# Kernel optimization log

Hardware: AMD Instinct MI355X
Metric: run time of the kernel (lower is better)

## Reference

```python
import jax
import jax.numpy as jnp
import numpy as np
from jax import lax
from jax.scipy.special import logsumexp

B, T, D = 8, 512, 768
S, H, O = 8, 32, 32
TRANS_W, EMISS_W = 0.5, 0.5


def setup_inputs() -> dict:
    key = jax.random.key(0)
    ks = jax.random.split(key, 8)
    emb = jax.random.normal(ks[0], (B, T, D), dtype=jnp.float32)
    u = jax.random.uniform(ks[1], (B, T, S, O), minval=1e-3, maxval=1.0)
    obs = (u / u.sum(-1, keepdims=True)).astype(jnp.float32)
    seq_lengths = jax.random.randint(ks[2], (B,), T // 2, T + 1).at[0].set(T).astype(jnp.int32)
    # HMM params (match torch init)
    priors = jnp.zeros(H).at[0].set(1.0) + jnp.full(H, 0.001).at[0].set(0.0)
    priors = jnp.full(H, 0.001).at[0].set(1.0)
    state_priors = jnp.log(priors)
    unnorm_trans = jax.random.normal(ks[3], (H, H))
    unnorm_emiss = jnp.zeros((S, H, O))
    # xavier_uniform with relu gain
    gain = np.sqrt(2.0)
    a_t = gain * np.sqrt(6.0 / (D + H * H))
    Wt = jax.random.uniform(ks[4], (D, H * H), minval=-a_t, maxval=a_t)
    bt = jnp.zeros(H * H)
    a_e = gain * np.sqrt(6.0 / (D + H * O))
    We = jax.random.uniform(ks[5], (S, D, H * O), minval=-a_e, maxval=a_e)
    be = jnp.zeros((S, H * O))
    return {"emb": emb, "obs": obs, "seq_lengths": seq_lengths,
            "state_priors": state_priors, "unnorm_trans": unnorm_trans,
            "unnorm_emiss": unnorm_emiss, "Wt": Wt, "bt": bt, "We": We, "be": be}


def _chmm_forward(emb, obs, state_priors, unnorm_trans, unnorm_emiss, Wt, bt, We, be, seq_lengths):
    b, t, d = emb.shape
    s, h, o = unnorm_emiss.shape
    lsp = jax.nn.log_softmax(state_priors)                               # [H]
    trans = jax.nn.softmax(unnorm_trans, axis=-1)                        # [H,H]
    emiss = jax.nn.softmax(unnorm_emiss, axis=-1)                        # [S,H,O]
    nn_trans = jax.nn.softmax((emb @ Wt + bt).reshape(b, t, h, h), axis=-1)
    nn_emiss = jax.nn.softmax((jnp.einsum('btd,sde->btse', emb, We) + be).reshape(b, t, s, h, o), axis=-1)
    log_trans = jnp.log((1.0 - TRANS_W) * trans + TRANS_W * nn_trans)    # [B,T,H,H]
    log_emiss = jnp.log((1.0 - EMISS_W) * emiss + EMISS_W * nn_emiss)    # [B,T,S,H,O]

    # normalize_observation: replace non-observing sources on entity positions
    lbs = jnp.argmax(obs, axis=-1)                                       # [B,T,S]
    entity = lbs.sum(-1) > 0                                             # [B,T]
    no_ent = lbs == 0                                                    # [B,T,S]
    mask = entity[:, :, None] & no_ent
    subst = jnp.full((o,), 0.99 / o).at[0].set(0.01)
    obs = jnp.where(mask[..., None], subst, obs)

    # log emission probs: logsumexp over obs dim, sum over sources -> [B,T,H]
    lep = logsumexp(log_emiss + jnp.log(obs)[:, :, :, None, :], axis=-1).sum(axis=2)

    # forward recursion (normalized alpha), scan over time
    a0 = lsp + lep[:, 0]
    a0 = a0 - logsumexp(a0, axis=-1, keepdims=True)
    lep_t = jnp.swapaxes(lep, 0, 1)          # [T,B,H]
    tr_t = jnp.swapaxes(log_trans, 0, 1)     # [T,B,H,H]

    def fstep(a, x):
        lep_i, tr_i = x
        la = lep_i + logsumexp(a[:, :, None] + tr_i, axis=1)
        la = la - logsumexp(la, axis=-1, keepdims=True)
        return la, la

    _, alphas = lax.scan(fstep, a0, (lep_t[1:], tr_t[1:]))
    log_alpha = jnp.swapaxes(jnp.concatenate([a0[None], alphas], 0), 0, 1)   # [B,T,H]

    # backward recursion (reverse scan); uses lep at time t (faithful to source)
    def bstep(bv, x):
        lep_i, tr_i = x
        nb = logsumexp(tr_i + (lep_i + bv)[:, None, :], axis=-1)
        return nb, nb

    _, betas = lax.scan(bstep, jnp.zeros((b, h)), (lep_t[:-1], tr_t[:-1]), reverse=True)
    log_beta = jnp.swapaxes(jnp.concatenate([betas, jnp.zeros((1, b, h))], 0), 0, 1)  # [B,T,H]
    shifts = seq_lengths - t
    log_beta = jax.vmap(lambda bb, ss: jnp.roll(bb, ss, axis=0))(log_beta, shifts)

    log_gamma = log_alpha + log_beta
    ng = log_gamma - logsumexp(log_gamma, axis=-1, keepdims=True)
    # xi for t = 1..T-1 (vectorized, no recursion)
    xi = log_trans[:, 1:] + log_alpha[:, :-1, :, None] + (lep[:, 1:] + log_beta[:, 1:])[:, :, None, :]
    xi = xi - logsumexp(xi.reshape(b, t - 1, -1), axis=-1)[..., None, None]

    log_prior = (jnp.exp(ng[:, 0]) * lsp).sum(-1).mean()
    tran_terms = (jnp.exp(xi) * log_trans[:, 1:]).sum((-2, -1))          # [B,T-1]
    t1 = jnp.arange(t - 1)[None, :]
    log_tran = jnp.where(t1 < (seq_lengths - 1)[:, None], tran_terms, 0.0).sum(-1).mean()
    emis_terms = (jnp.exp(ng) * lep).sum(-1)                             # [B,T]
    t2 = jnp.arange(t)[None, :]
    log_emis = jnp.where(t2 < seq_lengths[:, None], emis_terms, 0.0).sum(-1).mean()
    ll = log_prior + log_tran + log_emis
    return ll, log_trans, log_emiss


def reference(emb, obs, seq_lengths, state_priors, unnorm_trans, unnorm_emiss, Wt, bt, We, be):
    return _chmm_forward(emb, obs, state_priors, unnorm_trans, unnorm_emiss, Wt, bt, We, be, seq_lengths)
```

## Files before the change

### kernel.cpp

```cpp
#include <hip/hip_runtime.h>
#include <hip/hip_bf16.h>


typedef __attribute__((ext_vector_type(8))) short bf16x8;
typedef __attribute__((ext_vector_type(4))) float f32x4;

#define B_MBF   0
#define B_LDOT  16777216
#define B_CHNK  16777216
#define B_ABND  18874368
#define B_BBND  18907136
#define B_PART  18939904
#define B_LEP   20971520
#define B_ELEP  21496064
#define B_ALIN  22020352
#define B_BLIN  22544640
#define B_TRSM  23068928
#define B_EMSM  23073024
#define B_OBSM  23105792
#define B_ABF   27447552
#define B_WTBF  33739008

#define OUT_TR_BASE 1
#define OUT_EM_BASE 4194305

__device__ __forceinline__ float wsum32(float v) {
#pragma unroll
  for (int m = 16; m >= 1; m >>= 1) v += __shfl_xor(v, m);
  return v;
}
__device__ __forceinline__ float wmax32(float v) {
#pragma unroll
  for (int m = 16; m >= 1; m >>= 1) v = fmaxf(v, __shfl_xor(v, m));
  return v;
}
__device__ __forceinline__ short f2bf(float f) {
  union { float f; unsigned int u; } c; c.f = f;
  unsigned int u = c.u;
  unsigned int r = (u + 0x7FFFu + ((u >> 16) & 1u)) >> 16;
  return (short)r;
}
__device__ __forceinline__ float bf2f(short h) {
  union { unsigned int u; float f; } c;
  c.u = ((unsigned int)(unsigned short)h) << 16;
  return c.f;
}
__device__ __forceinline__ void gload16(const void* g, void* l) {
  __builtin_amdgcn_global_load_lds(
      (const __attribute__((address_space(1))) unsigned int*)g,
      (__attribute__((address_space(3))) unsigned int*)l, 16, 0, 0);
}

__global__ __launch_bounds__(256) void k_prep(
    const float* __restrict__ emb, short* __restrict__ Abf,
    const float* __restrict__ Wt, const float* __restrict__ We,
    short* __restrict__ WT,
    const float* __restrict__ ut, const float* __restrict__ ue,
    float* __restrict__ tsm, float* __restrict__ esm,
    const float* __restrict__ obs, float* __restrict__ om) {
  __shared__ float tile[32][33];
  __shared__ int lbs_s[8];
  __shared__ int entf;
  const int blk = blockIdx.x;
  const int tid = threadIdx.x;
  if (blk < 3072) {
    const int idx = (blk * 256 + tid) * 4;
#pragma unroll
    for (int c = 0; c < 4; ++c) Abf[idx + c] = f2bf(emb[idx + c]);
  } else if (blk < 9984) {
    const int x = blk - 3072;
    const int nb = (x % 288) * 32, kb = (x / 288) * 32;
    const int tx = tid & 31, ty = tid >> 5;
#pragma unroll
    for (int ii = 0; ii < 4; ++ii) {
      const int k = kb + ty + ii * 8;
      const int n = nb + tx;
      float v;
      if (n < 1024) v = Wt[(size_t)k * 1024 + n];
      else {
        const int ne = n - 1024, s = ne >> 10, c = ne & 1023;
        v = We[((size_t)s * 768 + k) * 1024 + c];
      }
      tile[ty + ii * 8][tx] = v;
    }
    __syncthreads();
#pragma unroll
    for (int ii = 0; ii < 4; ++ii) {
      const int n = nb + ty + ii * 8;
      const int k = kb + tx;
      WT[(size_t)n * 768 + k] = f2bf(tile[tx][ty + ii * 8]);
    }
  } else if (blk < 14080) {
    const int bt = blk - 9984;
    const int o = tid & 31;
    const float v = obs[((size_t)bt << 8) + tid];
    float bv = v; int am = o;
#pragma unroll
    for (int m = 16; m >= 1; m >>= 1) {
      const float ov_ = __shfl_xor(bv, m);
      const int oa = __shfl_xor(am, m);
      if (ov_ > bv || (ov_ == bv && oa < am)) { bv = ov_; am = oa; }
    }
    if (o == 0) lbs_s[tid >> 5] = am;
    __syncthreads();
    if (tid == 0) {
      int e = 0;
#pragma unroll
      for (int s = 0; s < 8; ++s) e += lbs_s[s];
      entf = (e > 0) ? 1 : 0;
    }
    __syncthreads();
    const bool msk = entf && (lbs_s[tid >> 5] == 0);
    const float sub = (o == 0) ? 0.01f : (0.99f / 32.0f);
    om[((size_t)bt << 8) + tid] = msk ? sub : v;
  } else {
    const int row = (blk - 14080) * 8 + (tid >> 5);
    const int j = tid & 31;
    const float* src; float* dst;
    if (row < 32) { src = ut + row * 32; dst = tsm + row * 32; }
    else          { src = ue + (row - 32) * 32; dst = esm + (row - 32) * 32; }
    float v = src[j];
    float mx = wmax32(v);
    float e = __expf(v - mx);
    float s = wsum32(e);
    dst[j] = e / s;
  }
}

#define BM 128
#define BN 128
#define BK 64

__global__ __launch_bounds__(512, 4) void gemm_epi(
    const short* __restrict__ A, const short* __restrict__ WT,
    const float* __restrict__ btb, const float* __restrict__ beb,
    const float* __restrict__ tsm, const float* __restrict__ esm,
    const float* __restrict__ om,
    float* __restrict__ out, short* __restrict__ Mbf, float* __restrict__ ldot) {
  __shared__ __align__(16) char smem[32768];
  short* lsA = (short*)smem;
  short* lsB = (short*)(smem + 16384);
  float* lsOm = (float*)smem;

  const int bid = blockIdx.x;
  const int xcd = bid & 7;
  const int local = bid >> 3;
  const int ntile = xcd * 9 + (local % 9);
  const int mtile = local / 9;
  const int m0 = mtile * BM;
  const int n0 = ntile * BN;

  const int tid = threadIdx.x;
  const int lane = tid & 63;
  const int w = tid >> 6;
  const int wr = w >> 1, wc = w & 1;
  const int l15 = lane & 15, lq = lane >> 4;

  const int lr = lane >> 3;
  const int lc = (lane & 7) ^ lr;
  const short* gA = A + (size_t)(m0 + (w << 3) + lr) * 768 + (lc << 3);
  const short* gB = WT + (size_t)(n0 + (w << 3) + lr) * 768 + (lc << 3);
  const int lofs = (w << 10) + (lane << 4);
  char* lA = (char*)lsA + lofs;
  char* lB = (char*)lsB + lofs;

  f32x4 acc[2][4] = {};

  for (int kt = 0; kt < 768; kt += BK) {
#pragma unroll
    for (int it = 0; it < 2; ++it) {
      gload16(gA + it * (64 * 768) + kt, lA + (it << 13));
      gload16(gB + it * (64 * 768) + kt, lB + (it << 13));
    }
    __syncthreads();
#pragma unroll
    for (int kk = 0; kk < 2; ++kk) {
      const int kbyte = kk * 64 + lq * 16;
      bf16x8 af[2], bfr[4];
#pragma unroll
      for (int mi = 0; mi < 2; ++mi) {
        const int m = wr * 32 + mi * 16 + l15;
        af[mi] = *(const bf16x8*)((const char*)lsA + ((m * 128 + kbyte) ^ ((m & 7) << 4)));
      }
#pragma unroll
      for (int ni = 0; ni < 4; ++ni) {
        const int n = wc * 64 + ni * 16 + l15;
        bfr[ni] = *(const bf16x8*)((const char*)lsB + ((n * 128 + kbyte) ^ ((n & 7) << 4)));
      }
#pragma unroll
      for (int mi = 0; mi < 2; ++mi)
#pragma unroll
        for (int ni = 0; ni < 4; ++ni)
          acc[mi][ni] = __builtin_amdgcn_mfma_f32_16x16x32_bf16(af[mi], bfr[ni], acc[mi][ni], 0, 0, 0);
    }
    __syncthreads();
  }

  const bool isem = (n0 >= 1024);
  int sblk = 0;
  if (isem) {
    sblk = (n0 - 1024) >> 10;
    const int row = tid >> 2, part = (tid & 3) << 3;
    const float* src = om + (((size_t)(m0 + row)) << 8) + (sblk << 5) + part;
    float* dst = lsOm + row * 36 + part;
    *(float4*)dst = *(const float4*)src;
    *(float4*)(dst + 4) = *(const float4*)(src + 4);
    __syncthreads();
  }

#pragma unroll
  for (int g = 0; g < 2; ++g) {
    const int nbase = n0 + wc * 64 + g * 32;
    const int c0 = nbase + l15;
    const int c1 = c0 + 16;
    const float bias0 = isem ? beb[c0 - 1024] : btb[c0];
    const float bias1 = isem ? beb[c1 - 1024] : btb[c1];
    const float base0 = isem ? esm[c0 - 1024] : tsm[c0];
    const float base1 = isem ? esm[c1 - 1024] : tsm[c1];
    const int h = (nbase >> 5) & 31;
#pragma unroll
    for (int mi = 0; mi < 2; ++mi) {
      const int rl0 = wr * 32 + mi * 16 + lq * 4;
      const int rowb = m0 + rl0;
      float e0[4], e1[4], sm[4];
#pragma unroll
      for (int r = 0; r < 4; ++r) {
        e0[r] = __expf(acc[mi][2 * g][r] + bias0);
        e1[r] = __expf(acc[mi][2 * g + 1][r] + bias1);
        sm[r] = e0[r] + e1[r];
      }
#pragma unroll
      for (int m_ = 1; m_ < 16; m_ <<= 1) {
#pragma unroll
        for (int r = 0; r < 4; ++r) sm[r] += __shfl_xor(sm[r], m_);
      }
      float M0[4], M1[4], lg0[4], lg1[4];
#pragma unroll
      for (int r = 0; r < 4; ++r) {
        const float inv = 0.5f * __builtin_amdgcn_rcpf(sm[r]);
        M0[r] = 0.5f * base0 + e0[r] * inv;
        M1[r] = 0.5f * base1 + e1[r] * inv;
        lg0[r] = __logf(M0[r]);
        lg1[r] = __logf(M1[r]);
      }
      if (!isem) {
#pragma unroll
        for (int r = 0; r < 4; ++r) {
          const size_t rb = ((size_t)(rowb + r)) << 10;
          out[OUT_TR_BASE + rb + c0] = lg0[r];
          out[OUT_TR_BASE + rb + c1] = lg1[r];
          Mbf[rb + c0] = f2bf(M0[r]);
          Mbf[rb + c1] = f2bf(M1[r]);
        }
      } else {
        const int ne0 = c0 - 1024;
        float dt[4];
#pragma unroll
        for (int r = 0; r < 4; ++r) {
          const float* ov = lsOm + (rl0 + r) * 36;
          dt[r] = M0[r] * ov[l15] + M1[r] * ov[l15 + 16];
        }
#pragma unroll
        for (int m_ = 1; m_ < 16; m_ <<= 1) {
#pragma unroll
          for (int r = 0; r < 4; ++r) dt[r] += __shfl_xor(dt[r], m_);
        }
#pragma unroll
        for (int r = 0; r < 4; ++r) {
          const size_t rb = ((size_t)(rowb + r)) << 13;
          out[OUT_EM_BASE + rb + ne0] = lg0[r];
          out[OUT_EM_BASE + rb + ne0 + 16] = lg1[r];
        }
        if (l15 == 0) {
#pragma unroll
          for (int r = 0; r < 4; ++r)
            ldot[(((size_t)(rowb + r)) << 8) + (sblk << 5) + h] = __logf(dt[r]);
        }
      }
    }
  }
}

__global__ __launch_bounds__(64) void k_elep(const float* __restrict__ ldot,
                                             float* __restrict__ lep,
                                             float* __restrict__ elep) {
  const int bt = blockIdx.x;
  const int l = threadIdx.x, i = l & 31;
  const float* ld = ldot + ((size_t)bt << 8);
  float v = 0.f;
#pragma unroll
  for (int s = 0; s < 8; ++s) v += ld[(s << 5) + i];
  float mx = wmax32(v);
  if (l < 32) {
    lep[((size_t)bt << 5) + i] = v;
    elep[((size_t)bt << 5) + i] = __expf(v - mx);
  }
}

__global__ __launch_bounds__(256) void k_chunk(const short* __restrict__ Mbf,
                                               const float* __restrict__ elep,
                                               float* __restrict__ chnk) {
  const int blk = blockIdx.x;
  const int dir = blk >> 8;
  const int b = (blk >> 5) & 7, c = blk & 31;
  int t0, t1;
  if (dir == 0) { t0 = 16 * c + 1; t1 = 16 * c + 16; if (t1 > 511) t1 = 511; }
  else          { t0 = 16 * c;     t1 = 16 * c + 15; if (t1 > 510) t1 = 510; }
  const size_t base = (size_t)b << 9;
  __shared__ float Pl[1024];
  __shared__ float Gl[1024];
  __shared__ float red[4];
  const int tid = threadIdx.x;
  const int r = tid >> 3;
  const int cq = (tid & 7) << 2;
  float4 p;
  {
    const short4 mh = *(const short4*)(Mbf + ((base + t0) << 10) + (tid << 2));
    const float4 e = *(const float4*)(elep + ((base + t0) << 5) + cq);
    p.x = bf2f(mh.x) * e.x; p.y = bf2f(mh.y) * e.y;
    p.z = bf2f(mh.z) * e.z; p.w = bf2f(mh.w) * e.w;
  }
  for (int t = t0 + 1; t <= t1; ++t) {
    *(float4*)(Pl + (tid << 2)) = p;
    const short4 mh = *(const short4*)(Mbf + ((base + t) << 10) + (tid << 2));
    const float4 e = *(const float4*)(elep + ((base + t) << 5) + cq);
    float4 g;
    g.x = bf2f(mh.x) * e.x; g.y = bf2f(mh.y) * e.y;
    g.z = bf2f(mh.z) * e.z; g.w = bf2f(mh.w) * e.w;
    *(float4*)(Gl + (tid << 2)) = g;
    __syncthreads();
    float4 nv = {0.f, 0.f, 0.f, 0.f};
#pragma unroll
    for (int j = 0; j < 32; ++j) {
      const float pr = Pl[(r << 5) + j];
      const float4 gj = *(const float4*)(Gl + (j << 5) + cq);
      nv.x = fmaf(pr, gj.x, nv.x);
      nv.y = fmaf(pr, gj.y, nv.y);
      nv.z = fmaf(pr, gj.z, nv.z);
      nv.w = fmaf(pr, gj.w, nv.w);
    }
    float mx = fmaxf(fmaxf(nv.x, nv.y), fmaxf(nv.z, nv.w));
#pragma unroll
    for (int mm = 32; mm >= 1; mm >>= 1) mx = fmaxf(mx, __shfl_xor(mx, mm));
    if ((tid & 63) == 0) red[tid >> 6] = mx;
    __syncthreads();
    mx = fmaxf(fmaxf(red[0], red[1]), fmaxf(red[2], red[3]));
    const float rs = __builtin_amdgcn_rcpf(mx);
    p.x = nv.x * rs; p.y = nv.y * rs; p.z = nv.z * rs; p.w = nv.w * rs;
  }
  *(float4*)(chnk + ((size_t)blk << 10) + (tid << 2)) = p;
}

__global__ __launch_bounds__(64) void k_stitch(const float* __restrict__ chnk,
                                               const float* __restrict__ elep,
                                               const float* __restrict__ sp,
                                               float* __restrict__ ab,
                                               float* __restrict__ bb) {
  const int l = threadIdx.x, i = l & 31, half = l >> 5;
  const int bid = blockIdx.x;
  const int b = bid & 7;
  float v;
  float pb0[16], pb1[16];
  if (bid < 8) {
    const float* base = chnk + ((size_t)(b << 5) << 10);
    auto LDP = [&](float (&pb)[16], int c) {
      const float* P = base + ((size_t)c << 10) + ((half << 4) << 5) + i;
#pragma unroll
      for (int jj = 0; jj < 16; ++jj) pb[jj] = P[jj << 5];
    };
    auto STEP = [&](float (&pb)[16], int c) {
      float pj[16];
#pragma unroll
      for (int jj = 0; jj < 16; ++jj) pj[jj] = __shfl(v, (half << 4) + jj);
      float a0 = 0.f, a1 = 0.f, a2 = 0.f, a3 = 0.f;
#pragma unroll
      for (int q = 0; q < 4; ++q) {
        a0 = fmaf(pj[(q << 2) + 0], pb[(q << 2) + 0], a0);
        a1 = fmaf(pj[(q << 2) + 1], pb[(q << 2) + 1], a1);
        a2 = fmaf(pj[(q << 2) + 2], pb[(q << 2) + 2], a2);
        a3 = fmaf(pj[(q << 2) + 3], pb[(q << 2) + 3], a3);
      }
      float av = (a0 + a1) + (a2 + a3);
      av += __shfl_xor(av, 32);
      const float S = wsum32(av);
      v = av * __builtin_amdgcn_rcpf(S);
      if (l < 32) ab[(((b << 5) + (c + 1)) << 5) + i] = v;
    };
    {
      float u = sp[i];
      float mx = wmax32(u);
      float pe = __expf(u - mx);
      float s = wsum32(pe);
      v = (pe / s) * elep[((size_t)(b << 9) << 5) + i];
      float S = wsum32(v);
      v /= S;
      if (l < 32) ab[((b << 5) << 5) + i] = v;
    }
    LDP(pb0, 0);
    int c = 0;
    for (; c + 1 <= 30; c += 2) {
      LDP(pb1, c + 1);
      STEP(pb0, c);
      LDP(pb0, (c + 2 <= 30) ? c + 2 : 30);
      STEP(pb1, c + 1);
    }
    if (c == 30) STEP(pb0, 30);
  } else {
    const float* base = chnk + ((size_t)(256 + (b << 5)) << 10);
    auto LDP = [&](float (&pb)[16], int c) {
      const float4* P = (const float4*)(base + ((size_t)c << 10) + (i << 5) + (half << 4));
#pragma unroll
      for (int q = 0; q < 4; ++q) {
        const float4 x = P[q];
        pb[(q << 2) + 0] = x.x; pb[(q << 2) + 1] = x.y;
        pb[(q << 2) + 2] = x.z; pb[(q << 2) + 3] = x.w;
      }
    };
    auto STEP = [&](float (&pb)[16], int c) {
      float qj[16];
#pragma unroll
      for (int jj = 0; jj < 16; ++jj) qj[jj] = __shfl(v, (half << 4) + jj);
      float a0 = 0.f, a1 = 0.f, a2 = 0.f, a3 = 0.f;
#pragma unroll
      for (int q = 0; q < 4; ++q) {
        a0 = fmaf(qj[(q << 2) + 0], pb[(q << 2) + 0], a0);
        a1 = fmaf(qj[(q << 2) + 1], pb[(q << 2) + 1], a1);
        a2 = fmaf(qj[(q << 2) + 2], pb[(q << 2) + 2], a2);
        a3 = fmaf(qj[(q << 2) + 3], pb[(q << 2) + 3], a3);
      }
      float av = (a0 + a1) + (a2 + a3);
      av += __shfl_xor(av, 32);
      const float S = wsum32(av);
      v = av * __builtin_amdgcn_rcpf(S);
      if (l < 32) bb[(((b << 5) + c) << 5) + i] = v;
    };
    v = 1.0f / 32.0f;
    LDP(pb0, 31);
    int c = 31;
    for (; c - 1 >= 1; c -= 2) {
      LDP(pb1, c - 1);
      STEP(pb0, c);
      LDP(pb0, (c - 2 >= 1) ? c - 2 : 1);
      STEP(pb1, c - 1);
    }
    if (c == 1) STEP(pb0, 1);
  }
}

__global__ __launch_bounds__(64) void k_recon(const short* __restrict__ Mbf,
                                              const float* __restrict__ elep,
                                              const float* __restrict__ ab,
                                              const float* __restrict__ bb,
                                              float* __restrict__ alin,
                                              float* __restrict__ blin) {
  const int l = threadIdx.x, i = l & 31, half = l >> 5;
  const int blk = blockIdx.x;
  const int dir = blk >> 8;
  const int b = (blk >> 5) & 7, c = blk & 31;
  const size_t base = (size_t)b << 9;
  const short* Mb = Mbf + (base << 10);
  const float* Eb = elep + (base << 5);
  float v;
  float m0[16], m1[16];
  float e0, e1;
  if (dir == 0) {
    float* Ab = alin + (base << 5);
    const int cb = ((half << 4) << 5) + i;
    auto LDF = [&](float (&mb)[16], float& eb, int t) {
      const short* Mr = Mb + ((size_t)t << 10) + cb;
#pragma unroll
      for (int jj = 0; jj < 16; ++jj) mb[jj] = bf2f(Mr[jj << 5]);
      eb = Eb[(t << 5) + i];
    };
    auto STEPF = [&](float (&mb)[16], float eb, int t) {
      float pj[16];
#pragma unroll
      for (int jj = 0; jj < 16; ++jj) pj[jj] = __shfl(v, (half << 4) + jj);
      float a0 = 0.f, a1 = 0.f, a2 = 0.f, a3 = 0.f;
#pragma unroll
      for (int q = 0; q < 4; ++q) {
        a0 = fmaf(pj[(q << 2) + 0], mb[(q << 2) + 0], a0);
        a1 = fmaf(pj[(q << 2) + 1], mb[(q << 2) + 1], a1);
        a2 = fmaf(pj[(q << 2) + 2], mb[(q << 2) + 2], a2);
        a3 = fmaf(pj[(q << 2) + 3], mb[(q << 2) + 3], a3);
      }
      float av = (a0 + a1) + (a2 + a3);
      av += __shfl_xor(av, 32);
      const float nv = av * eb;
      const float S = wsum32(nv);
      v = nv * __builtin_amdgcn_rcpf(S);
      if (l < 32) Ab[(t << 5) + i] = v;
    };
    v = ab[(((b << 5) + c) << 5) + i];
    const int t0 = c << 4;
    if (l < 32) Ab[(t0 << 5) + i] = v;
    const int te = t0 + 15;
    LDF(m0, e0, t0 + 1);
    int t = t0 + 1;
    for (; t + 1 <= te; t += 2) {
      LDF(m1, e1, t + 1);
      STEPF(m0, e0, t);
      LDF(m0, e0, (t + 2 <= te) ? t + 2 : te);
      STEPF(m1, e1, t + 1);
    }
    if (t == te) STEPF(m0, e0, t);
  } else {
    float* Bb = blin + (base << 5);
    auto LDB = [&](float (&mb)[16], float& eb, int t) {
      const short4* Mr = (const short4*)(Mb + ((size_t)t << 10) + (i << 5) + (half << 4));
#pragma unroll
      for (int q = 0; q < 4; ++q) {
        const short4 x = Mr[q];
        mb[(q << 2) + 0] = bf2f(x.x); mb[(q << 2) + 1] = bf2f(x.y);
        mb[(q << 2) + 2] = bf2f(x.z); mb[(q << 2) + 3] = bf2f(x.w);
      }
      eb = Eb[(t << 5) + i];
    };
    auto STEPB = [&](float (&mb)[16], float eb, int t) {
      const float q0 = v * eb;
      float qj[16];
#pragma unroll
      for (int jj = 0; jj < 16; ++jj) qj[jj] = __shfl(q0, (half << 4) + jj);
      float a0 = 0.f, a1 = 0.f, a2 = 0.f, a3 = 0.f;
#pragma unroll
      for (int q = 0; q < 4; ++q) {
        a0 = fmaf(qj[(q << 2) + 0], mb[(q << 2) + 0], a0);
        a1 = fmaf(qj[(q << 2) + 1], mb[(q << 2) + 1], a1);
        a2 = fmaf(qj[(q << 2) + 2], mb[(q << 2) + 2], a2);
        a3 = fmaf(qj[(q << 2) + 3], mb[(q << 2) + 3], a3);
      }
      float av = (a0 + a1) + (a2 + a3);
      av += __shfl_xor(av, 32);
      const float S = wsum32(av);
      v = av * __builtin_amdgcn_rcpf(S);
      if (l < 32) Bb[(t << 5) + i] = v;
    };
    int ts;
    if (c == 31) {
      v = 1.0f / 32.0f;
      if (l < 32) Bb[(511 << 5) + i] = v;
      ts = 510;
    } else {
      v = bb[(((b << 5) + (c + 1)) << 5) + i];
      ts = (c << 4) + 15;
    }
    const int te = c << 4;
    LDB(m0, e0, ts);
    int t = ts;
    for (; t - 1 >= te; t -= 2) {
      LDB(m1, e1, t - 1);
      STEPB(m0, e0, t);
      LDB(m0, e0, (t - 2 >= te) ? t - 2 : te);
      STEPB(m1, e1, t - 1);
    }
    if (t == te) STEPB(m0, e0, t);
  }
}

__global__ __launch_bounds__(64) void k_final(
    const float* __restrict__ out_log,
    const float* __restrict__ alin, const float* __restrict__ blin,
    const float* __restrict__ elep, const float* __restrict__ lep,
    const int* __restrict__ seqlen, const float* __restrict__ sp,
    float* __restrict__ part) {
  const int bt = blockIdx.x;
  const int b = bt >> 9, t = bt & 511;
  const int l = threadIdx.x, i = l & 31;
  const int L = seqlen[b];
  const int tb = (t + 512 - L) & 511;
  const float a = alin[((size_t)bt << 5) + i];
  const float br = blin[((((size_t)b << 9) + tb) << 5) + i];
  const float g = a * br;
  float Z = wsum32(g);
  Z = fmaxf(Z, 1e-37f);
  const float ng = g / Z;
  const float es = wsum32(ng * lep[((size_t)bt << 5) + i]);
  float pr = 0.0f;
  if (t == 0) {
    const float v = sp[i];
    const float mx = wmax32(v);
    const float pe = __expf(v - mx);
    const float ss = wsum32(pe);
    const float lsp = v - mx - __logf(ss);
    pr = wsum32(ng * lsp);
  }
  float tran = 0.0f;
  if (t >= 1) {
    const float u = elep[((size_t)bt << 5) + i] * br;
    const int jb = (l & 1) << 4;
    float uj[16];
#pragma unroll
    for (int jj = 0; jj < 16; ++jj) uj[jj] = __shfl(u, jb + jj);
    const float ap = alin[(((size_t)bt - 1) << 5) + (l >> 1)];
    const float* Lr = out_log + OUT_TR_BASE + ((size_t)bt << 10) + ((l >> 1) << 5) + jb;
    float accZ = 0.0f, accT = 0.0f;
#pragma unroll
    for (int c = 0; c < 16; ++c) {
      const float lv = Lr[c];
      const float wv = __expf(lv) * ap * uj[c];
      accZ += wv;
      accT = fmaf(wv, lv, accT);
    }
#pragma unroll
    for (int m_ = 32; m_ >= 1; m_ >>= 1) {
      accZ += __shfl_xor(accZ, m_);
      accT += __shfl_xor(accT, m_);
    }
    tran = accT / accZ;
  }
  if (l == 0) {
    part[bt * 3 + 0] = (t == 0) ? pr : 0.0f;
    part[bt * 3 + 1] = (t >= 1 && t < L) ? tran : 0.0f;
    part[bt * 3 + 2] = (t < L) ? es : 0.0f;
  }
}

__global__ __launch_bounds__(256) void k_ll(const float* __restrict__ part,
                                            float* __restrict__ out) {
  __shared__ float red[8];
  const int tid = threadIdx.x;
  const int b = tid >> 5, i = tid & 31;
  float s = 0.0f;
#pragma unroll
  for (int k = 0; k < 16; ++k) {
    const int bt = (b << 9) + (k << 5) + i;
    s += part[bt * 3 + 0] + part[bt * 3 + 1] + part[bt * 3 + 2];
  }
  s = wsum32(s);
  if (i == 0) red[b] = s;
  __syncthreads();
  if (tid == 0) {
    float v = 0.0f;
#pragma unroll
    for (int b2 = 0; b2 < 8; ++b2) v += red[b2];
    out[0] = v / 8.0f;
  }
}

extern "C" void kernel_launch(void* const* d_in, const int* in_sizes, int n_in,
                              void* d_out, int out_size, void* d_ws, size_t ws_size,
                              hipStream_t stream) {
  const float* emb    = (const float*)d_in[0];
  const float* obs    = (const float*)d_in[1];
  const int*   seqlen = (const int*)  d_in[2];
  const float* sp     = (const float*)d_in[3];
  const float* utr    = (const float*)d_in[4];
  const float* uem    = (const float*)d_in[5];
  const float* Wt     = (const float*)d_in[6];
  const float* btb    = (const float*)d_in[7];
  const float* We     = (const float*)d_in[8];
  const float* beb    = (const float*)d_in[9];
  float* out = (float*)d_out;
  char* ws = (char*)d_ws;

  short* Mbf  = (short*)(ws + B_MBF);
  float* ldot = (float*)(ws + B_LDOT);
  float* chnk = (float*)(ws + B_CHNK);
  float* abnd = (float*)(ws + B_ABND);
  float* bbnd = (float*)(ws + B_BBND);
  float* part = (float*)(ws + B_PART);
  float* lep  = (float*)(ws + B_LEP);
  float* elep = (float*)(ws + B_ELEP);
  float* alin = (float*)(ws + B_ALIN);
  float* blin = (float*)(ws + B_BLIN);
  float* tsm  = (float*)(ws + B_TRSM);
  float* esm  = (float*)(ws + B_EMSM);
  float* om   = (float*)(ws + B_OBSM);
  short* Abf  = (short*)(ws + B_ABF);
  short* WTbf = (short*)(ws + B_WTBF);

  k_prep<<<14116, 256, 0, stream>>>(emb, Abf, Wt, We, WTbf, utr, uem, tsm, esm,
                                    obs, om);
  gemm_epi<<<2304, 512, 0, stream>>>(Abf, WTbf, btb, beb, tsm, esm, om,
                                     out, Mbf, ldot);
  k_elep<<<4096, 64, 0, stream>>>(ldot, lep, elep);
  k_chunk<<<512, 256, 0, stream>>>(Mbf, elep, chnk);
  k_stitch<<<16, 64, 0, stream>>>(chnk, elep, sp, abnd, bbnd);
  k_recon<<<512, 64, 0, stream>>>(Mbf, elep, abnd, bbnd, alin, blin);
  k_final<<<4096, 64, 0, stream>>>(out, alin, blin, elep, lep, seqlen, sp, part);
  k_ll<<<1, 256, 0, stream>>>(part, out);
}
```

Baseline: 164.1 us.

## Triple-buffer GEMM K-loop with BK=32 and async prefetch two stages ahead

Replaces the single-buffered BK=64 GEMM main loop, which synchronized twice per iteration, with a three-stage LDS ring buffer using BK=32. Loads are issued two stages ahead, and a single barrier per step is guarded by explicit vmcnt waits. The LDS layout and swizzle are reworked so each half-tile row pair maps conflict-free, with offsets precomputed outside the loop. The aim is to overlap global-to-LDS copies with MFMA work. In exchange it uses 48KB of shared memory, which may limit occupancy, and it doubles the number of loop iterations.

```diff
diff --git a/kernel.cpp b/kernel.cpp
--- a/kernel.cpp
+++ b/kernel.cpp
@@ -129,7 +129,7 @@
 
 #define BM 128
 #define BN 128
-#define BK 64
+#define BK 32
 
 __global__ __launch_bounds__(512, 4) void gemm_epi(
     const short* __restrict__ A, const short* __restrict__ WT,
@@ -137,9 +137,7 @@
     const float* __restrict__ tsm, const float* __restrict__ esm,
     const float* __restrict__ om,
     float* __restrict__ out, short* __restrict__ Mbf, float* __restrict__ ldot) {
-  __shared__ __align__(16) char smem[32768];
-  short* lsA = (short*)smem;
-  short* lsB = (short*)(smem + 16384);
+  __shared__ __align__(16) char smem[49152];
   float* lsOm = (float*)smem;
 
   const int bid = blockIdx.x;
@@ -156,44 +154,60 @@
   const int wr = w >> 1, wc = w & 1;
   const int l15 = lane & 15, lq = lane >> 4;
 
-  const int lr = lane >> 3;
-  const int lc = (lane & 7) ^ lr;
-  const short* gA = A + (size_t)(m0 + (w << 3) + lr) * 768 + (lc << 3);
-  const short* gB = WT + (size_t)(n0 + (w << 3) + lr) * 768 + (lc << 3);
+  const int jh = (lane & 7) ^ (lane >> 3);
+  const int srow = (w << 4) + ((lane >> 3) << 1) + (jh & 1);
+  const int sc = jh >> 1;
+  const short* gA = A + (size_t)(m0 + srow) * 768 + (sc << 3);
+  const short* gB = WT + (size_t)(n0 + srow) * 768 + (sc << 3);
   const int lofs = (w << 10) + (lane << 4);
-  char* lA = (char*)lsA + lofs;
-  char* lB = (char*)lsB + lofs;
+
+  int offA[2], offB[4];
+#pragma unroll
+  for (int mi = 0; mi < 2; ++mi) {
+    const int r = wr * 32 + mi * 16 + l15;
+    offA[mi] = ((r >> 1) << 7) + (((((r & 1)) + (lq << 1)) ^ ((r >> 1) & 7)) << 4);
+  }
+#pragma unroll
+  for (int ni = 0; ni < 4; ++ni) {
+    const int r = wc * 64 + ni * 16 + l15;
+    offB[ni] = 8192 + (((r >> 1)) << 7) + ((((r & 1) + (lq << 1)) ^ ((r >> 1) & 7)) << 4);
+  }
 
   f32x4 acc[2][4] = {};
 
-  for (int kt = 0; kt < 768; kt += BK) {
-#pragma unroll
-    for (int it = 0; it < 2; ++it) {
-      gload16(gA + it * (64 * 768) + kt, lA + (it << 13));
-      gload16(gB + it * (64 * 768) + kt, lB + (it << 13));
-    }
-    __syncthreads();
-#pragma unroll
-    for (int kk = 0; kk < 2; ++kk) {
-      const int kbyte = kk * 64 + lq * 16;
-      bf16x8 af[2], bfr[4];
-#pragma unroll
-      for (int mi = 0; mi < 2; ++mi) {
-        const int m = wr * 32 + mi * 16 + l15;
-        af[mi] = *(const bf16x8*)((const char*)lsA + ((m * 128 + kbyte) ^ ((m & 7) << 4)));
-      }
-#pragma unroll
-      for (int ni = 0; ni < 4; ++ni) {
-        const int n = wc * 64 + ni * 16 + l15;
-        bfr[ni] = *(const bf16x8*)((const char*)lsB + ((n * 128 + kbyte) ^ ((n & 7) << 4)));
-      }
-#pragma unroll
-      for (int mi = 0; mi < 2; ++mi)
-#pragma unroll
-        for (int ni = 0; ni < 4; ++ni)
-          acc[mi][ni] = __builtin_amdgcn_mfma_f32_16x16x32_bf16(af[mi], bfr[ni], acc[mi][ni], 0, 0, 0);
-    }
-    __syncthreads();
+  auto STAGE = [&](int bi, int kt) {
+    char* d = smem + (bi << 14) + lofs;
+    gload16(gA + kt, d);
+    gload16(gB + kt, d + 8192);
+  };
+
+  STAGE(0, 0);
+  STAGE(1, 32);
+  asm volatile("s_waitcnt vmcnt(2)" ::: "memory");
+  __builtin_amdgcn_s_barrier();
+  __builtin_amdgcn_sched_barrier(0);
+
+  int b0 = 0, b1 = 1, b2 = 2;
+#pragma unroll 3
+  for (int it = 0; it < 24; ++it) {
+    if (it < 22) STAGE(b2, (it + 2) * 32);
+    const char* s = smem + (b0 << 14);
+    bf16x8 af[2], bfr[4];
+#pragma unroll
+    for (int mi = 0; mi < 2; ++mi) af[mi] = *(const bf16x8*)(s + offA[mi]);
+#pragma unroll
+    for (int ni = 0; ni < 4; ++ni) bfr[ni] = *(const bf16x8*)(s + offB[ni]);
+#pragma unroll
+    for (int mi = 0; mi < 2; ++mi)
+#pragma unroll
+      for (int ni = 0; ni < 4; ++ni)
+        acc[mi][ni] = __builtin_amdgcn_mfma_f32_16x16x32_bf16(af[mi], bfr[ni], acc[mi][ni], 0, 0, 0);
+    if (it < 22)      asm volatile("s_waitcnt vmcnt(2)" ::: "memory");
+    else if (it < 23) asm volatile("s_waitcnt vmcnt(0)" ::: "memory");
+    __builtin_amdgcn_sched_barrier(0);
+    __builtin_amdgcn_s_barrier();
+    __builtin_amdgcn_sched_barrier(0);
+    const int tb = b0; b0 = b1; b1 = b2; b2 = tb;
   }
 
   const bool isem = (n0 >= 1024);
```

Measured after the change: 171.8 us. 1.05x slower.
